# Kernel optimization log

Measured on AMD Instinct MI355X. Metric: run time of the kernel, lower is better.

The kernel has to match this reference:

```python
import jax, jax.numpy as jnp
import numpy as np

# module hyper-parameters (VoronoiDecoder defaults)
S = 256          # n_seeds
Q = 262144       # query uv points
EPS = 1e-8
W_MIN = 0.005
BETA = 0.02
RAW_TEMP = 5.0
H_MIN, H_MAX = 0.5, 2.0
J_BETA_SCALE = 1.0
J_WIDTH_BONUS = 0.15
J_KEFF_K0 = 3.0
J_KEFF_S = 0.35
J_TRIPLE_LAMBDA = 0.15
J_TRIPLE_POWER = 1.5
KNN_K = 8
SOFTMIN_TAU = 0.002


def setup_inputs() -> dict:
    key = jax.random.key(0)
    ks = jax.random.split(key, 7)
    return {
        "uv": jax.random.uniform(ks[0], (Q, 2), jnp.float32),
        "seeds_raw": jax.random.uniform(ks[1], (S, 2), jnp.float32),
        "w_raw": jax.random.normal(ks[2], (S, S), jnp.float32),
        "h_raw": jax.random.normal(ks[3], (S,), jnp.float32),
        "theta": jax.random.normal(ks[4], (S,), jnp.float32),
        "a_raw": 0.3 * jax.random.normal(ks[5], (S,), jnp.float32),
        "seed_gates": jax.random.normal(ks[6], (S,), jnp.float32),
    }


def reference(uv, seeds_raw, w_raw, h_raw, theta, a_raw, seed_gates):
    seeds = seeds_raw  # seeds_uv is identity

    # --- pairwise seed distances (default buffers: all faces non-periodic,
    # seed_face_id all zero -> periodic wrap is a no-op -> plain euclidean) ---
    pd = jnp.linalg.norm(seeds[None, :, :] - seeds[:, None, :], axis=-1)  # (S,S)
    w_max_pair = jnp.maximum(0.8 * pd, W_MIN + EPS)
    w_geo = W_MIN + (w_max_pair - W_MIN) * jax.nn.sigmoid(w_raw / RAW_TEMP)
    W = 0.5 * (w_geo + w_geo.T)  # symmetric pairwise wall widths (S,S)

    h = H_MIN + (H_MAX - H_MIN) * jax.nn.sigmoid(h_raw)  # (S,) heights
    gates = jax.nn.sigmoid(seed_gates)                    # (S,) seed gates

    # --- anisotropic (unit-determinant) metric distance per seed ---
    c, sn = jnp.cos(theta), jnp.sin(theta)
    sc = jnp.exp(a_raw)  # anisotropy scale per seed
    dx = uv[:, None, 0] - seeds[None, :, 0]  # (Q,S)
    dy = uv[:, None, 1] - seeds[None, :, 1]
    xp = (c * dx + sn * dy) / sc   # rotate into seed frame, scale axes
    yp = (-sn * dx + c * dy) * sc
    d = jnp.sqrt(xp * xp + yp * yp + EPS)  # (Q,S) metric distances

    # --- kNN over seeds ---
    negk, idx = jax.lax.top_k(-d, KNN_K)   # (Q,K)
    dk = -negk
    d1, d3 = dk[:, 0], dk[:, 2]
    i1, i2 = idx[:, 0], idx[:, 1]
    w_pair = W[i1, i2]  # width of the wall between the 2 nearest cells

    # --- junction effects via softmin cell-membership weights ---
    p = jax.nn.softmax(-d / (BETA * J_BETA_SCALE), axis=-1)  # (Q,S)
    k_eff = 1.0 / (jnp.sum(p * p, axis=-1) + EPS)            # effective #cells
    bonus = J_WIDTH_BONUS * jax.nn.sigmoid((k_eff - J_KEFF_K0) / J_KEFF_S)
    triple = J_TRIPLE_LAMBDA * jnp.exp(-((d3 - d1) / (w_pair + EPS)) ** J_TRIPLE_POWER)
    w_eff = w_pair * (1.0 + bonus + triple)

    # --- softmin distance to Voronoi boundary over kNN bisectors ---
    b = 0.5 * (dk[:, 1:] - d1[:, None])  # (Q,K-1) bisector half-gaps
    sdist = -SOFTMIN_TAU * jax.nn.logsumexp(-b / SOFTMIN_TAU, axis=-1)
    wall = jax.nn.sigmoid((0.5 * w_eff - sdist) / BETA)  # shell occupancy

    h_blend = p @ h        # (Q,) blended height
    g_blend = p @ gates    # (Q,) blended gate
    return wall * g_blend * h_blend
```

## Files before the change

### kernel.cpp

```cpp
#include <hip/hip_runtime.h>

#define NSEED 256
#define KBF 72.13475204444817f
#define INV_KB 0.013862943611198906f

typedef float v2f __attribute__((ext_vector_type(2)));
typedef float v16f __attribute__((ext_vector_type(16)));

__device__ __forceinline__ float fast_exp(float x) {
  return __builtin_amdgcn_exp2f(x * 1.4426950408889634f);
}
__device__ __forceinline__ float sigf(float x) {
  return 1.0f / (1.0f + fast_exp(-x));
}
__device__ __forceinline__ float med3(float x, float lo, float hi) {
  return __builtin_amdgcn_fmed3f(x, lo, hi);
}
__device__ __forceinline__ v2f vfma(v2f a, v2f b, v2f c) {
  return __builtin_elementwise_fma(a, b, c);
}

__global__ void seed_setup_kernel(const float* __restrict__ seeds,
                                  const float* __restrict__ h_raw,
                                  const float* __restrict__ theta,
                                  const float* __restrict__ a_raw,
                                  const float* __restrict__ seed_gates,
                                  float* __restrict__ Pg) {
  int s = threadIdx.x;
  if (s >= NSEED) return;
  float sx = seeds[2 * s], sy = seeds[2 * s + 1];
  float th = theta[s];
  float c = cosf(th), sn = sinf(th);
  float sc = expf(a_raw[s]);
  float inv = 1.0f / sc;
  float h = 0.5f + 1.5f * sigf(h_raw[s]);
  float g = sigf(seed_gates[s]);
  float A11 = KBF * c * inv, A12 = KBF * sn * inv;
  float A21 = -KBF * sn * sc, A22 = KBF * c * sc;
  float TX = -(A11 * sx + A12 * sy);
  float TY = -(A21 * sx + A22 * sy);
  float* base = Pg + (s >> 1) * 16;
  int b = s & 1;
  base[0 + b] = A11;
  base[2 + b] = A12;
  base[4 + b] = A21;
  base[6 + b] = A22;
  base[8 + b] = TX;
  base[10 + b] = TY;
  base[12 + b] = h;
  base[14 + b] = g;
}

__global__ __launch_bounds__(256, 8) void voronoi_kernel(
    const float* __restrict__ uv, const float* __restrict__ seeds,
    const float* __restrict__ w_raw, const float* __restrict__ Pg,
    float* __restrict__ out, int nq) {
  __shared__ float LD[2][14][64];

  const int wid = threadIdx.x >> 6;
  const int lane = threadIdx.x & 63;
  const int grp = wid >> 1;
  const int half = wid & 1;
  const int shalf = __builtin_amdgcn_readfirstlane(half);
  const int q = blockIdx.x * 128 + grp * 64 + lane;
  const int qc = q < nq ? q : nq - 1;
  const float2 uvq = ((const float2*)uv)[qc];
  const v2f uu = {uvq.x, uvq.x}, vv = {uvq.y, uvq.y};
  const v2f epsS = {1e-8f * KBF * KBF, 1e-8f * KBF * KBF};

  float dk0 = 3e38f, dk1 = 3e38f, dk2 = 3e38f, dk3 = 3e38f;
  float dk4 = 3e38f, dk5 = 3e38f, dk6 = 3e38f, dk7 = 3e38f;
  int i0 = 0, i1 = 0;
  v2f S1 = {0.f, 0.f}, S2 = {0.f, 0.f}, Sh = {0.f, 0.f}, Sg = {0.f, 0.f};

#define INS(x, sidx)             \
  {                              \
    float _d = (x);              \
    bool c0 = _d < dk0;          \
    bool c1 = _d < dk1;          \
    int sh = c0 ? i0 : (sidx);   \
    i1 = c1 ? sh : i1;           \
    i0 = c0 ? (sidx) : i0;       \
    dk7 = med3(_d, dk6, dk7);    \
    dk6 = med3(_d, dk5, dk6);    \
    dk5 = med3(_d, dk4, dk5);    \
    dk4 = med3(_d, dk3, dk4);    \
    dk3 = med3(_d, dk2, dk3);    \
    dk2 = med3(_d, dk1, dk2);    \
    dk1 = med3(_d, dk0, dk1);    \
    dk0 = fminf(_d, dk0);        \
  }

  const v16f* __restrict__ PG = (const v16f*)(Pg + shalf * 1024);
#pragma unroll 4
  for (int k = 0; k < 64; ++k) {
    v16f P = PG[k];
    v2f A11 = {P[0], P[1]}, A12 = {P[2], P[3]};
    v2f A21 = {P[4], P[5]}, A22 = {P[6], P[7]};
    v2f TX = {P[8], P[9]}, TY = {P[10], P[11]};
    v2f hh = {P[12], P[13]}, gg = {P[14], P[15]};
    v2f xp = vfma(A11, uu, vfma(A12, vv, TX));
    v2f yp = vfma(A21, uu, vfma(A22, vv, TY));
    v2f d2 = vfma(xp, xp, vfma(yp, yp, epsS));
    INS(d2.x, 2 * k)
    INS(d2.y, 2 * k + 1)
    float da = __builtin_amdgcn_sqrtf(d2.x);
    float db = __builtin_amdgcn_sqrtf(d2.y);
    v2f e;
    e.x = __builtin_amdgcn_exp2f(-da);
    e.y = __builtin_amdgcn_exp2f(-db);
    S1 += e;
    S2 = vfma(e, e, S2);
    Sh = vfma(e, hh, Sh);
    Sg = vfma(e, gg, Sg);
  }
#undef INS

  i0 |= shalf << 7;
  i1 |= shalf << 7;

  float S1s = S1.x + S1.y;
  float S2s = S2.x + S2.y;
  float Shs = Sh.x + Sh.y;
  float Sgs = Sg.x + Sg.y;

  if (half == 1) {
    LD[grp][0][lane] = dk0;
    LD[grp][1][lane] = dk1;
    LD[grp][2][lane] = dk2;
    LD[grp][3][lane] = dk3;
    LD[grp][4][lane] = dk4;
    LD[grp][5][lane] = dk5;
    LD[grp][6][lane] = dk6;
    LD[grp][7][lane] = dk7;
    LD[grp][8][lane] = __int_as_float(i0);
    LD[grp][9][lane] = __int_as_float(i1);
    LD[grp][10][lane] = S1s;
    LD[grp][11][lane] = S2s;
    LD[grp][12][lane] = Shs;
    LD[grp][13][lane] = Sgs;
  }
  __syncthreads();
  if (half == 1 || q >= nq) return;

  float b0 = LD[grp][0][lane], b1 = LD[grp][1][lane];
  float b2 = LD[grp][2][lane], b3 = LD[grp][3][lane];
  float b4 = LD[grp][4][lane], b5 = LD[grp][5][lane];
  float b6 = LD[grp][6][lane], b7 = LD[grp][7][lane];
  int j0 = __float_as_int(LD[grp][8][lane]);
  int j1 = __float_as_int(LD[grp][9][lane]);
  S1s += LD[grp][10][lane];
  S2s += LD[grp][11][lane];
  Shs += LD[grp][12][lane];
  Sgs += LD[grp][13][lane];

  bool aw = b0 < dk0;
  float ec1 = aw ? dk0 : dk1;
  int ic1 = aw ? i0 : i1;
  float ec2 = aw ? b1 : b0;
  int ic2 = aw ? j1 : j0;
  const int I0 = aw ? j0 : i0;
  const int I1 = (ec2 < ec1) ? ic2 : ic1;

  float m0 = fminf(dk0, b7), m1 = fminf(dk1, b6);
  float m2 = fminf(dk2, b5), m3 = fminf(dk3, b4);
  float m4 = fminf(dk4, b3), m5 = fminf(dk5, b2);
  float m6 = fminf(dk6, b1), m7 = fminf(dk7, b0);
#define CE(a, b)             \
  {                          \
    float _lo = fminf(a, b); \
    float _hi = fmaxf(a, b); \
    a = _lo;                 \
    b = _hi;                 \
  }
  CE(m0, m4) CE(m1, m5) CE(m2, m6) CE(m3, m7)
  CE(m0, m2) CE(m1, m3) CE(m4, m6) CE(m5, m7)
  CE(m0, m1) CE(m2, m3) CE(m4, m5) CE(m6, m7)
#undef CE

  float e0 = __builtin_amdgcn_sqrtf(m0);
  float e1 = __builtin_amdgcn_sqrtf(m1);
  float e2 = __builtin_amdgcn_sqrtf(m2);
  float e3 = __builtin_amdgcn_sqrtf(m3);
  float e4 = __builtin_amdgcn_sqrtf(m4);
  float e5 = __builtin_amdgcn_sqrtf(m5);
  float e6 = __builtin_amdgcn_sqrtf(m6);
  float e7 = __builtin_amdgcn_sqrtf(m7);

  float ax = seeds[2 * I0], ay = seeds[2 * I0 + 1];
  float bx = seeds[2 * I1], by = seeds[2 * I1 + 1];
  float pdx = ax - bx, pdy = ay - by;
  float pd = __builtin_amdgcn_sqrtf(fmaf(pdx, pdx, pdy * pdy));
  float wmax = fmaxf(0.8f * pd, 0.005f + 1e-8f);
  float wr01 = w_raw[(I0 << 8) + I1];
  float wr10 = w_raw[(I1 << 8) + I0];
  float w_pair = 0.005f + (wmax - 0.005f) * 0.5f * (sigf(wr01 * 0.2f) + sigf(wr10 * 0.2f));

  float s1sq = S1s * S1s;
  float keff = s1sq / fmaf(1e-8f, s1sq, S2s);
  float bonus = 0.15f * sigf((keff - 3.0f) * (1.0f / 0.35f));

  float tt = (e2 - e0) * INV_KB / (w_pair + 1e-8f);
  float t15 = tt * __builtin_amdgcn_sqrtf(tt);
  float triple = 0.15f * fast_exp(-t15);

  float w_eff = w_pair * (1.0f + bonus + triple);

  float acc = 1.0f;
  acc += __builtin_amdgcn_exp2f((e1 - e2) * 5.0f);
  acc += __builtin_amdgcn_exp2f((e1 - e3) * 5.0f);
  acc += __builtin_amdgcn_exp2f((e1 - e4) * 5.0f);
  acc += __builtin_amdgcn_exp2f((e1 - e5) * 5.0f);
  acc += __builtin_amdgcn_exp2f((e1 - e6) * 5.0f);
  acc += __builtin_amdgcn_exp2f((e1 - e7) * 5.0f);
  float b1s = (e1 - e0) * (0.5f * INV_KB);
  float sdist = b1s - 0.002f * 0.6931471805599453f * __builtin_amdgcn_logf(acc);

  float wall = sigf((0.5f * w_eff - sdist) * 50.0f);
  float invS1 = 1.0f / S1s;
  out[q] = wall * (Sgs * invS1) * (Shs * invS1);
}

extern "C" void kernel_launch(void* const* d_in, const int* in_sizes, int n_in,
                              void* d_out, int out_size, void* d_ws, size_t ws_size,
                              hipStream_t stream) {
  (void)in_sizes;
  (void)n_in;
  (void)ws_size;
  const float* uv = (const float*)d_in[0];
  const float* seeds = (const float*)d_in[1];
  const float* w_raw = (const float*)d_in[2];
  const float* h_raw = (const float*)d_in[3];
  const float* theta = (const float*)d_in[4];
  const float* a_raw = (const float*)d_in[5];
  const float* gates = (const float*)d_in[6];
  float* out = (float*)d_out;
  float* Pg = (float*)d_ws;

  seed_setup_kernel<<<1, 256, 0, stream>>>(seeds, h_raw, theta, a_raw, gates, Pg);
  int nq = out_size;
  long long threads = 2LL * nq;
  int grid = (int)((threads + 255) / 256);
  voronoi_kernel<<<grid, 256, 0, stream>>>(uv, seeds, w_raw, Pg, out, nq);
}
```

Measured before the change: 114.7 us.

## Bin queries into grid cells and prune seeds per cell with distance bounds

Adds a 32x32 spatial grid over the query domain. One kernel builds a candidate seed list per cell: seeds that can enter the top-8 first, then seeds whose softmax weight could still matter within a margin. Queries are counting-sorted into cells with histogram, scan and scatter kernels, and the main kernel then evaluates only each cell's candidate seeds instead of all 256. This cuts the per-query distance and exp work, at the cost of several extra launches, atomics, and an approximation that drops seeds with negligible softmax weight; the old kernel is kept as a fallback when the workspace is too small.

```diff
diff --git a/kernel.cpp b/kernel.cpp
--- a/kernel.cpp
+++ b/kernel.cpp
@@ -3,6 +3,23 @@
 #define NSEED 256
 #define KBF 72.13475204444817f
 #define INV_KB 0.013862943611198906f
+#define EPSSC 5.20342e-5f
+#define RKSC 1.5945f
+#define MSC 20.1977f
+#define FPM 1e-3f
+
+#define OFF_PG 0u
+#define OFF_PS 8192u
+#define OFF_SIG 16384u
+#define OFF_SMAX 17408u
+#define OFF_LENT 17472u
+#define OFF_LENS 21568u
+#define OFF_LIST 25664u
+#define OFF_QCNT 1074240u
+#define OFF_QOFF 1078336u
+#define OFF_QCUR 1082432u
+#define OFF_PERM 1086528u
+#define WS_NEED 2135104u
 
 typedef float v2f __attribute__((ext_vector_type(2)));
 typedef float v16f __attribute__((ext_vector_type(16)));
@@ -20,60 +37,134 @@
   return __builtin_elementwise_fma(a, b, c);
 }
 
-__global__ void seed_setup_kernel(const float* __restrict__ seeds,
-                                  const float* __restrict__ h_raw,
-                                  const float* __restrict__ theta,
-                                  const float* __restrict__ a_raw,
-                                  const float* __restrict__ seed_gates,
-                                  float* __restrict__ Pg) {
+__global__ void setup_kernel(const float* __restrict__ seeds,
+                             const float* __restrict__ h_raw,
+                             const float* __restrict__ theta,
+                             const float* __restrict__ a_raw,
+                             const float* __restrict__ gates,
+                             float* __restrict__ Pg, float* __restrict__ Ps,
+                             float* __restrict__ Sig, float* __restrict__ Smax) {
+  __shared__ float red[256];
   int s = threadIdx.x;
-  if (s >= NSEED) return;
   float sx = seeds[2 * s], sy = seeds[2 * s + 1];
   float th = theta[s];
   float c = cosf(th), sn = sinf(th);
   float sc = expf(a_raw[s]);
   float inv = 1.0f / sc;
   float h = 0.5f + 1.5f * sigf(h_raw[s]);
-  float g = sigf(seed_gates[s]);
+  float g = sigf(gates[s]);
   float A11 = KBF * c * inv, A12 = KBF * sn * inv;
   float A21 = -KBF * sn * sc, A22 = KBF * c * sc;
   float TX = -(A11 * sx + A12 * sy);
   float TY = -(A21 * sx + A22 * sy);
-  float* base = Pg + (s >> 1) * 16;
-  int b = s & 1;
-  base[0 + b] = A11;
-  base[2 + b] = A12;
-  base[4 + b] = A21;
-  base[6 + b] = A22;
-  base[8 + b] = TX;
-  base[10 + b] = TY;
-  base[12 + b] = h;
-  base[14 + b] = g;
-}
-
-__global__ __launch_bounds__(256, 8) void voronoi_kernel(
-    const float* __restrict__ uv, const float* __restrict__ seeds,
-    const float* __restrict__ w_raw, const float* __restrict__ Pg,
-    float* __restrict__ out, int nq) {
-  __shared__ float LD[2][14][64];
-
-  const int wid = threadIdx.x >> 6;
-  const int lane = threadIdx.x & 63;
-  const int grp = wid >> 1;
-  const int half = wid & 1;
-  const int shalf = __builtin_amdgcn_readfirstlane(half);
-  const int q = blockIdx.x * 128 + grp * 64 + lane;
-  const int qc = q < nq ? q : nq - 1;
-  const float2 uvq = ((const float2*)uv)[qc];
-  const v2f uu = {uvq.x, uvq.x}, vv = {uvq.y, uvq.y};
-  const v2f epsS = {1e-8f * KBF * KBF, 1e-8f * KBF * KBF};
-
+  {
+    float* base = Pg + (s >> 1) * 16;
+    int b = s & 1;
+    base[0 + b] = A11; base[2 + b] = A12;
+    base[4 + b] = A21; base[6 + b] = A22;
+    base[8 + b] = TX;  base[10 + b] = TY;
+    base[12 + b] = h;  base[14 + b] = g;
+  }
+  float* P = Ps + s * 8;
+  P[0] = A11; P[1] = A12; P[2] = A21; P[3] = A22;
+  P[4] = TX;  P[5] = TY;  P[6] = h;   P[7] = g;
+  float sig = fmaxf(sc, inv);
+  Sig[s] = sig;
+  red[s] = sig;
+  __syncthreads();
+  for (int off = 128; off > 0; off >>= 1) {
+    if (s < off) red[s] = fmaxf(red[s], red[s + off]);
+    __syncthreads();
+  }
+  if (s == 0) Smax[0] = red[0];
+}
+
+__global__ __launch_bounds__(256) void cell_kernel(
+    const float* __restrict__ Ps, const float* __restrict__ Sig,
+    const float* __restrict__ Smax, unsigned* __restrict__ lenT,
+    unsigned* __restrict__ lenS, unsigned* __restrict__ list) {
+  const int cell = blockIdx.x * 256 + threadIdx.x;
+  const float cx = ((cell & 31) + 0.5f) * (1.0f / 32.0f);
+  const float cy = ((cell >> 5) + 0.5f) * (1.0f / 32.0f);
+  const float sbar = Smax[0];
   float dk0 = 3e38f, dk1 = 3e38f, dk2 = 3e38f, dk3 = 3e38f;
   float dk4 = 3e38f, dk5 = 3e38f, dk6 = 3e38f, dk7 = 3e38f;
-  int i0 = 0, i1 = 0;
-  v2f S1 = {0.f, 0.f}, S2 = {0.f, 0.f}, Sh = {0.f, 0.f}, Sg = {0.f, 0.f};
-
-#define INS(x, sidx)             \
+  for (int s = 0; s < NSEED; ++s) {
+    const float* P = Ps + s * 8;
+    float xp = fmaf(P[0], cx, fmaf(P[1], cy, P[4]));
+    float yp = fmaf(P[2], cx, fmaf(P[3], cy, P[5]));
+    float d2 = fmaf(xp, xp, fmaf(yp, yp, EPSSC));
+    dk7 = med3(d2, dk6, dk7); dk6 = med3(d2, dk5, dk6);
+    dk5 = med3(d2, dk4, dk5); dk4 = med3(d2, dk3, dk4);
+    dk3 = med3(d2, dk2, dk3); dk2 = med3(d2, dk1, dk2);
+    dk1 = med3(d2, dk0, dk1); dk0 = fminf(d2, dk0);
+  }
+  const float D8 = __builtin_amdgcn_sqrtf(dk7);
+  const float d1c = __builtin_amdgcn_sqrtf(dk0);
+  const float base2 = fmaxf(d1c + MSC, D8);
+  unsigned* Lc = list + (cell << 8);
+  int n = 0;
+  for (int s = 0; s < NSEED; ++s) {
+    const float* P = Ps + s * 8;
+    float xp = fmaf(P[0], cx, fmaf(P[1], cy, P[4]));
+    float yp = fmaf(P[2], cx, fmaf(P[3], cy, P[5]));
+    float d2 = fmaf(xp, xp, fmaf(yp, yp, EPSSC));
+    float t = D8 + (Sig[s] + sbar) * RKSC + FPM;
+    if (d2 <= t * t) Lc[n++] = (unsigned)s;
+  }
+  const int nT = n;
+  for (int s = 0; s < NSEED; ++s) {
+    const float* P = Ps + s * 8;
+    float xp = fmaf(P[0], cx, fmaf(P[1], cy, P[4]));
+    float yp = fmaf(P[2], cx, fmaf(P[3], cy, P[5]));
+    float d2 = fmaf(xp, xp, fmaf(yp, yp, EPSSC));
+    float sl = (Sig[s] + sbar) * RKSC + FPM;
+    float t1 = D8 + sl, t2 = base2 + sl;
+    if (d2 > t1 * t1 && d2 <= t2 * t2) Lc[n++] = (unsigned)s;
+  }
+  lenT[cell] = (unsigned)nT;
+  lenS[cell] = (unsigned)n;
+}
+
+__global__ void hist_kernel(const float* __restrict__ uv,
+                            unsigned* __restrict__ qcnt, int nq) {
+  int q = blockIdx.x * 256 + threadIdx.x;
+  if (q >= nq) return;
+  float u = uv[2 * q], v = uv[2 * q + 1];
+  int ix = min(31, (int)(u * 32.0f)), iy = min(31, (int)(v * 32.0f));
+  atomicAdd(&qcnt[iy * 32 + ix], 1u);
+}
+
+__global__ void scan_kernel(const unsigned* __restrict__ qcnt,
+                            unsigned* __restrict__ qoff) {
+  __shared__ unsigned sc[1024];
+  int t = threadIdx.x;
+  unsigned myv = qcnt[t];
+  sc[t] = myv;
+  __syncthreads();
+  for (int off = 1; off < 1024; off <<= 1) {
+    unsigned v = (t >= off) ? sc[t - off] : 0u;
+    __syncthreads();
+    sc[t] += v;
+    __syncthreads();
+  }
+  qoff[t] = sc[t] - myv;
+}
+
+__global__ void scatter_kernel(const float* __restrict__ uv,
+                               const unsigned* __restrict__ qoff,
+                               unsigned* __restrict__ qcur,
+                               unsigned* __restrict__ perm, int nq) {
+  int q = blockIdx.x * 256 + threadIdx.x;
+  if (q >= nq) return;
+  float u = uv[2 * q], v = uv[2 * q + 1];
+  int ix = min(31, (int)(u * 32.0f)), iy = min(31, (int)(v * 32.0f));
+  int cell = iy * 32 + ix;
+  unsigned pos = qoff[cell] + atomicAdd(&qcur[cell], 1u);
+  perm[pos] = (unsigned)q;
+}
+
+#define INSF(x, sidx)            \
   {                              \
     float _d = (x);              \
     bool c0 = _d < dk0;          \
@@ -91,6 +182,112 @@
     dk0 = fminf(_d, dk0);        \
   }
 
+__global__ __launch_bounds__(256) void main_kernel(
+    const float* __restrict__ uv, const float* __restrict__ seeds,
+    const float* __restrict__ w_raw, const float* __restrict__ Ps,
+    const unsigned* __restrict__ lenT, const unsigned* __restrict__ lenS,
+    const unsigned* __restrict__ list, const unsigned* __restrict__ qcnt,
+    const unsigned* __restrict__ qoff, const unsigned* __restrict__ perm,
+    float* __restrict__ out) {
+  const int cell = blockIdx.x >> 2;
+  const int chunk = blockIdx.x & 3;
+  const int cnt = (int)qcnt[cell];
+  const int base = (int)qoff[cell];
+  const int nT = (int)lenT[cell];
+  const int nS = (int)lenS[cell];
+  const unsigned* Lc = list + (cell << 8);
+  for (int i = (chunk << 8) + threadIdx.x; i < cnt; i += 1024) {
+    const int q = (int)perm[base + i];
+    const float2 uq = ((const float2*)uv)[q];
+    const float u = uq.x, v = uq.y;
+    float dk0 = 3e38f, dk1 = 3e38f, dk2 = 3e38f, dk3 = 3e38f;
+    float dk4 = 3e38f, dk5 = 3e38f, dk6 = 3e38f, dk7 = 3e38f;
+    int i0 = 0, i1 = 0;
+    float S1 = 0.f, S2 = 0.f, Sh = 0.f, Sg = 0.f;
+    for (int j = 0; j < nT; ++j) {
+      int s = (int)__builtin_amdgcn_readfirstlane(Lc[j]);
+      const float* P = Ps + (s << 3);
+      float xp = fmaf(P[0], u, fmaf(P[1], v, P[4]));
+      float yp = fmaf(P[2], u, fmaf(P[3], v, P[5]));
+      float d2 = fmaf(xp, xp, fmaf(yp, yp, EPSSC));
+      INSF(d2, s)
+      float d = __builtin_amdgcn_sqrtf(d2);
+      float e = __builtin_amdgcn_exp2f(-d);
+      S1 += e;
+      S2 = fmaf(e, e, S2);
+      Sh = fmaf(e, P[6], Sh);
+      Sg = fmaf(e, P[7], Sg);
+    }
+    for (int j = nT; j < nS; ++j) {
+      int s = (int)__builtin_amdgcn_readfirstlane(Lc[j]);
+      const float* P = Ps + (s << 3);
+      float xp = fmaf(P[0], u, fmaf(P[1], v, P[4]));
+      float yp = fmaf(P[2], u, fmaf(P[3], v, P[5]));
+      float d2 = fmaf(xp, xp, fmaf(yp, yp, EPSSC));
+      float d = __builtin_amdgcn_sqrtf(d2);
+      float e = __builtin_amdgcn_exp2f(-d);
+      S1 += e;
+      S2 = fmaf(e, e, S2);
+      Sh = fmaf(e, P[6], Sh);
+      Sg = fmaf(e, P[7], Sg);
+    }
+    float e0 = __builtin_amdgcn_sqrtf(dk0);
+    float e1 = __builtin_amdgcn_sqrtf(dk1);
+    float e2 = __builtin_amdgcn_sqrtf(dk2);
+    float e3 = __builtin_amdgcn_sqrtf(dk3);
+    float e4 = __builtin_amdgcn_sqrtf(dk4);
+    float e5 = __builtin_amdgcn_sqrtf(dk5);
+    float e6 = __builtin_amdgcn_sqrtf(dk6);
+    float e7 = __builtin_amdgcn_sqrtf(dk7);
+    float ax = seeds[2 * i0], ay = seeds[2 * i0 + 1];
+    float bx = seeds[2 * i1], by = seeds[2 * i1 + 1];
+    float pdx = ax - bx, pdy = ay - by;
+    float pd = __builtin_amdgcn_sqrtf(fmaf(pdx, pdx, pdy * pdy));
+    float wmax = fmaxf(0.8f * pd, 0.005f + 1e-8f);
+    float wr01 = w_raw[(i0 << 8) + i1];
+    float wr10 = w_raw[(i1 << 8) + i0];
+    float w_pair = 0.005f + (wmax - 0.005f) * 0.5f * (sigf(wr01 * 0.2f) + sigf(wr10 * 0.2f));
+    float s1sq = S1 * S1;
+    float keff = s1sq / fmaf(1e-8f, s1sq, S2);
+    float bonus = 0.15f * sigf((keff - 3.0f) * (1.0f / 0.35f));
+    float tt = (e2 - e0) * INV_KB / (w_pair + 1e-8f);
+    float t15 = tt * __builtin_amdgcn_sqrtf(tt);
+    float triple = 0.15f * fast_exp(-t15);
+    float w_eff = w_pair * (1.0f + bonus + triple);
+    float acc = 1.0f;
+    acc += __builtin_amdgcn_exp2f((e1 - e2) * 5.0f);
+    acc += __builtin_amdgcn_exp2f((e1 - e3) * 5.0f);
+    acc += __builtin_amdgcn_exp2f((e1 - e4) * 5.0f);
+    acc += __builtin_amdgcn_exp2f((e1 - e5) * 5.0f);
+    acc += __builtin_amdgcn_exp2f((e1 - e6) * 5.0f);
+    acc += __builtin_amdgcn_exp2f((e1 - e7) * 5.0f);
+    float b1s = (e1 - e0) * (0.5f * INV_KB);
+    float sdist = b1s - 0.002f * 0.6931471805599453f * __builtin_amdgcn_logf(acc);
+    float wall = sigf((0.5f * w_eff - sdist) * 50.0f);
+    float invS1 = 1.0f / S1;
+    out[q] = wall * (Sg * invS1) * (Sh * invS1);
+  }
+}
+
+__global__ __launch_bounds__(256, 8) void fallback_kernel(
+    const float* __restrict__ uv, const float* __restrict__ seeds,
+    const float* __restrict__ w_raw, const float* __restrict__ Pg,
+    float* __restrict__ out, int nq) {
+  __shared__ float LD[2][14][64];
+  const int wid = threadIdx.x >> 6;
+  const int lane = threadIdx.x & 63;
+  const int grp = wid >> 1;
+  const int half = wid & 1;
+  const int shalf = __builtin_amdgcn_readfirstlane(half);
+  const int q = blockIdx.x * 128 + grp * 64 + lane;
+  const int qc = q < nq ? q : nq - 1;
+  const float2 uvq = ((const float2*)uv)[qc];
+  const v2f uu = {uvq.x, uvq.x}, vv = {uvq.y, uvq.y};
+  const v2f epsS = {EPSSC, EPSSC};
+  float dk0 = 3e38f, dk1 = 3e38f, dk2 = 3e38f, dk3 = 3e38f;
+  float dk4 = 3e38f, dk5 = 3e38f, dk6 = 3e38f, dk7 = 3e38f;
+  int i0 = 0, i1 = 0;
+  v2f S1 = {0.f, 0.f}, S2 = {0.f, 0.f}, Sh = {0.f, 0.f}, Sg = {0.f, 0.f};
   const v16f* __restrict__ PG = (const v16f*)(Pg + shalf * 1024);
 #pragma unroll 4
   for (int k = 0; k < 64; ++k) {
@@ -102,8 +299,8 @@
     v2f xp = vfma(A11, uu, vfma(A12, vv, TX));
     v2f yp = vfma(A21, uu, vfma(A22, vv, TY));
     v2f d2 = vfma(xp, xp, vfma(yp, yp, epsS));
-    INS(d2.x, 2 * k)
-    INS(d2.y, 2 * k + 1)
+    INSF(d2.x, 2 * k)
+    INSF(d2.y, 2 * k + 1)
     float da = __builtin_amdgcn_sqrtf(d2.x);
     float db = __builtin_amdgcn_sqrtf(d2.y);
     v2f e;
@@ -114,46 +311,30 @@
     Sh = vfma(e, hh, Sh);
     Sg = vfma(e, gg, Sg);
   }
-#undef INS
-
   i0 |= shalf << 7;
   i1 |= shalf << 7;
-
-  float S1s = S1.x + S1.y;
-  float S2s = S2.x + S2.y;
-  float Shs = Sh.x + Sh.y;
-  float Sgs = Sg.x + Sg.y;
-
+  float S1s = S1.x + S1.y, S2s = S2.x + S2.y;
+  float Shs = Sh.x + Sh.y, Sgs = Sg.x + Sg.y;
   if (half == 1) {
-    LD[grp][0][lane] = dk0;
-    LD[grp][1][lane] = dk1;
-    LD[grp][2][lane] = dk2;
-    LD[grp][3][lane] = dk3;
-    LD[grp][4][lane] = dk4;
-    LD[grp][5][lane] = dk5;
-    LD[grp][6][lane] = dk6;
-    LD[grp][7][lane] = dk7;
+    LD[grp][0][lane] = dk0; LD[grp][1][lane] = dk1;
+    LD[grp][2][lane] = dk2; LD[grp][3][lane] = dk3;
+    LD[grp][4][lane] = dk4; LD[grp][5][lane] = dk5;
+    LD[grp][6][lane] = dk6; LD[grp][7][lane] = dk7;
     LD[grp][8][lane] = __int_as_float(i0);
     LD[grp][9][lane] = __int_as_float(i1);
-    LD[grp][10][lane] = S1s;
-    LD[grp][11][lane] = S2s;
-    LD[grp][12][lane] = Shs;
-    LD[grp][13][lane] = Sgs;
+    LD[grp][10][lane] = S1s; LD[grp][11][lane] = S2s;
+    LD[grp][12][lane] = Shs; LD[grp][13][lane] = Sgs;
   }
   __syncthreads();
   if (half == 1 || q >= nq) return;
-
   float b0 = LD[grp][0][lane], b1 = LD[grp][1][lane];
   float b2 = LD[grp][2][lane], b3 = LD[grp][3][lane];
   float b4 = LD[grp][4][lane], b5 = LD[grp][5][lane];
   float b6 = LD[grp][6][lane], b7 = LD[grp][7][lane];
   int j0 = __float_as_int(LD[grp][8][lane]);
   int j1 = __float_as_int(LD[grp][9][lane]);
-  S1s += LD[grp][10][lane];
-  S2s += LD[grp][11][lane];
-  Shs += LD[grp][12][lane];
-  Sgs += LD[grp][13][lane];
-
+  S1s += LD[grp][10][lane]; S2s += LD[grp][11][lane];
+  Shs += LD[grp][12][lane]; Sgs += LD[grp][13][lane];
   bool aw = b0 < dk0;
   float ec1 = aw ? dk0 : dk1;
   int ic1 = aw ? i0 : i1;
@@ -161,7 +342,6 @@
   int ic2 = aw ? j1 : j0;
   const int I0 = aw ? j0 : i0;
   const int I1 = (ec2 < ec1) ? ic2 : ic1;
-
   float m0 = fminf(dk0, b7), m1 = fminf(dk1, b6);
   float m2 = fminf(dk2, b5), m3 = fminf(dk3, b4);
   float m4 = fminf(dk4, b3), m5 = fminf(dk5, b2);
@@ -177,7 +357,6 @@
   CE(m0, m2) CE(m1, m3) CE(m4, m6) CE(m5, m7)
   CE(m0, m1) CE(m2, m3) CE(m4, m5) CE(m6, m7)
 #undef CE
-
   float e0 = __builtin_amdgcn_sqrtf(m0);
   float e1 = __builtin_amdgcn_sqrtf(m1);
   float e2 = __builtin_amdgcn_sqrtf(m2);
@@ -186,7 +365,6 @@
   float e5 = __builtin_amdgcn_sqrtf(m5);
   float e6 = __builtin_amdgcn_sqrtf(m6);
   float e7 = __builtin_amdgcn_sqrtf(m7);
-
   float ax = seeds[2 * I0], ay = seeds[2 * I0 + 1];
   float bx = seeds[2 * I1], by = seeds[2 * I1 + 1];
   float pdx = ax - bx, pdy = ay - by;
@@ -195,17 +373,13 @@
   float wr01 = w_raw[(I0 << 8) + I1];
   float wr10 = w_raw[(I1 << 8) + I0];
   float w_pair = 0.005f + (wmax - 0.005f) * 0.5f * (sigf(wr01 * 0.2f) + sigf(wr10 * 0.2f));
-
   float s1sq = S1s * S1s;
   float keff = s1sq / fmaf(1e-8f, s1sq, S2s);
   float bonus = 0.15f * sigf((keff - 3.0f) * (1.0f / 0.35f));
-
   float tt = (e2 - e0) * INV_KB / (w_pair + 1e-8f);
   float t15 = tt * __builtin_amdgcn_sqrtf(tt);
   float triple = 0.15f * fast_exp(-t15);
-
   float w_eff = w_pair * (1.0f + bonus + triple);
-
   float acc = 1.0f;
   acc += __builtin_amdgcn_exp2f((e1 - e2) * 5.0f);
   acc += __builtin_amdgcn_exp2f((e1 - e3) * 5.0f);
@@ -215,7 +389,6 @@
   acc += __builtin_amdgcn_exp2f((e1 - e7) * 5.0f);
   float b1s = (e1 - e0) * (0.5f * INV_KB);
   float sdist = b1s - 0.002f * 0.6931471805599453f * __builtin_amdgcn_logf(acc);
-
   float wall = sigf((0.5f * w_eff - sdist) * 50.0f);
   float invS1 = 1.0f / S1s;
   out[q] = wall * (Sgs * invS1) * (Shs * invS1);
@@ -226,7 +399,6 @@
                               hipStream_t stream) {
   (void)in_sizes;
   (void)n_in;
-  (void)ws_size;
   const float* uv = (const float*)d_in[0];
   const float* seeds = (const float*)d_in[1];
   const float* w_raw = (const float*)d_in[2];
@@ -235,11 +407,37 @@
   const float* a_raw = (const float*)d_in[5];
   const float* gates = (const float*)d_in[6];
   float* out = (float*)d_out;
-  float* Pg = (float*)d_ws;
-
-  seed_setup_kernel<<<1, 256, 0, stream>>>(seeds, h_raw, theta, a_raw, gates, Pg);
-  int nq = out_size;
-  long long threads = 2LL * nq;
-  int grid = (int)((threads + 255) / 256);
-  voronoi_kernel<<<grid, 256, 0, stream>>>(uv, seeds, w_raw, Pg, out, nq);
-}
+  char* ws = (char*)d_ws;
+  const int nq = out_size;
+
+  float* Pg = (float*)(ws + OFF_PG);
+  float* Ps = (float*)(ws + OFF_PS);
+  float* Sig = (float*)(ws + OFF_SIG);
+  float* Smax = (float*)(ws + OFF_SMAX);
+
+  if (ws_size >= WS_NEED) {
+    unsigned* lenT = (unsigned*)(ws + OFF_LENT);
+    unsigned* lenS = (unsigned*)(ws + OFF_LENS);
+    unsigned* list = (unsigned*)(ws + OFF_LIST);
+    unsigned* qcnt = (unsigned*)(ws + OFF_QCNT);
+    unsigned* qoff = (unsigned*)(ws + OFF_QOFF);
+    unsigned* qcur = (unsigned*)(ws + OFF_QCUR);
+    unsigned* perm = (unsigned*)(ws + OFF_PERM);
+    hipMemsetAsync(ws + OFF_QCNT, 0, 12288, stream);
+    setup_kernel<<<1, 256, 0, stream>>>(seeds, h_raw, theta, a_raw, gates, Pg,
+                                        Ps, Sig, Smax);
+    cell_kernel<<<4, 256, 0, stream>>>(Ps, Sig, Smax, lenT, lenS, list);
+    int qgrid = (nq + 255) / 256;
+    hist_kernel<<<qgrid, 256, 0, stream>>>(uv, qcnt, nq);
+    scan_kernel<<<1, 1024, 0, stream>>>(qcnt, qoff);
+    scatter_kernel<<<qgrid, 256, 0, stream>>>(uv, qoff, qcur, perm, nq);
+    main_kernel<<<4096, 256, 0, stream>>>(uv, seeds, w_raw, Ps, lenT, lenS,
+                                          list, qcnt, qoff, perm, out);
+  } else {
+    setup_kernel<<<1, 256, 0, stream>>>(seeds, h_raw, theta, a_raw, gates, Pg,
+                                        Ps, Sig, Smax);
+    long long threads = 2LL * nq;
+    int grid = (int)((threads + 255) / 256);
+    fallback_kernel<<<grid, 256, 0, stream>>>(uv, seeds, w_raw, Pg, out, nq);
+  }
+}
```

Result: slower. 379.1 us (+230.4%).
